# Performance work log

Measured on AMD Instinct MI355X. Metric: run time of the kernel, lower is better.

The kernel has to match this reference:

```python
import jax, jax.numpy as jnp
import numpy as np

TQ, TV, B, D, UNITS = 256, 1024, 4, 128, 128
NEG_INF = -1e9


def setup_inputs() -> dict:
    key = jax.random.key(0)
    k1, k2, k3, k4, k5, k6 = jax.random.split(key, 6)
    query = jax.random.normal(k1, (TQ, B, D), dtype=jnp.float32)
    value = jax.random.normal(k2, (TV, B, D), dtype=jnp.float32)
    mask = jax.random.randint(k3, (TV, B), 0, 2).astype(bool)
    # guarantee at least one valid key position per batch element
    mask = mask.at[0].set(True)
    # Dense kernels (glorot-uniform-like scaled normals are fine for a reference)
    W1 = jax.random.normal(k4, (D, UNITS), dtype=jnp.float32) * (1.0 / np.sqrt(D))
    W2 = jax.random.normal(k5, (D, UNITS), dtype=jnp.float32) * (1.0 / np.sqrt(D))
    # AdditiveAttention use_scale=True -> learnable scale vector of shape (units,)
    scale = jax.random.normal(k6, (UNITS,), dtype=jnp.float32) * (1.0 / np.sqrt(UNITS))
    return {"query": query, "value": value, "mask": mask, "W1": W1, "W2": W2, "scale": scale}


def reference(query, value, mask, W1, W2, scale):
    # time-major -> batch-major
    q = jnp.transpose(query, (1, 0, 2))   # [B, Tq, D]
    v = jnp.transpose(value, (1, 0, 2))   # [B, Tv, D]
    m = jnp.transpose(mask, (1, 0))       # [B, Tv] bool (value mask)

    wq = jnp.einsum('bqd,du->bqu', q, W1)  # [B, Tq, U]
    wk = jnp.einsum('bvd,du->bvu', v, W2)  # [B, Tv, U]

    # additive score: sum_u scale[u] * tanh(wq[b,q,u] + wk[b,v,u]) -> [B, Tq, Tv]
    scores = jnp.einsum('u,bqvu->bqv', scale, jnp.tanh(wq[:, :, None, :] + wk[:, None, :, :]))

    scores = jnp.where(m[:, None, :], scores, NEG_INF)
    attn = jax.nn.softmax(scores, axis=-1)          # [B, Tq, Tv]
    ctx = jnp.einsum('bqv,bvd->bqd', attn, v)       # [B, Tq, D]

    # batch-major -> time-major
    return jnp.transpose(ctx, (1, 0, 2))            # [Tq, B, D]
```

## Files before the change

kernel.cpp:

```cpp
#include <hip/hip_runtime.h>


#define TQ 256
#define TV 1024
#define BB 4
#define DD 128
#define UU 128
#define NEG_INF -1e9f
#define C2LOG2E 2.8853900817779268f

__global__ __launch_bounds__(256) void compact_kernel(
    const int* __restrict__ mask,
    const float* __restrict__ scale,
    int* __restrict__ valid_idx,
    int* __restrict__ nvalid,
    float* __restrict__ Ssum)
{
    const int b = blockIdx.x;
    const int t = threadIdx.x, lane = t & 63, wid = t >> 6;
    __shared__ int wsum[4];
    __shared__ float sred[2];

    int m[4];
#pragma unroll
    for (int k = 0; k < 4; ++k) m[k] = mask[(4 * t + k) * BB + b] ? 1 : 0;
    int cnt = m[0] + m[1] + m[2] + m[3];

    int pre = cnt;
#pragma unroll
    for (int off = 1; off < 64; off <<= 1) {
        int y = __shfl_up(pre, off, 64);
        if (lane >= off) pre += y;
    }
    if (lane == 63) wsum[wid] = pre;

    float sv_ = (t < UU) ? scale[t] : 0.f;
#pragma unroll
    for (int off = 32; off > 0; off >>= 1) sv_ += __shfl_xor(sv_, off, 64);
    if (t == 0)  sred[0] = sv_;
    if (t == 64) sred[1] = sv_;
    __syncthreads();

    int base = 0;
#pragma unroll
    for (int w = 0; w < 4; ++w) if (w < wid) base += wsum[w];
    int total = wsum[0] + wsum[1] + wsum[2] + wsum[3];
    int idx = base + pre - cnt;

#pragma unroll
    for (int k = 0; k < 4; ++k)
        if (m[k]) valid_idx[b * TV + (idx++)] = 4 * t + k;
    for (int i = t; i < TV; i += 256)
        if (i >= total) valid_idx[b * TV + i] = 0;
    if (t == 0) nvalid[b] = total;
    if (b == 0 && t == 0) Ssum[0] = sred[0] + sred[1];
}

__global__ __launch_bounds__(256) void proj_all_kernel(
    const float* __restrict__ query, const float* __restrict__ value,
    const float* __restrict__ W1, const float* __restrict__ W2,
    float* __restrict__ Eq, float* __restrict__ Ek)
{
    __shared__ float Wl[DD * UU];
    __shared__ float xs[8][DD];
    const int t = threadIdx.x;

    const bool isq = blockIdx.x < (TQ * BB / 8);
    const float* X = isq ? query : value;
    const float* W = isq ? W1 : W2;
    float* out     = isq ? Eq : Ek;
    const int T    = isq ? TQ : TV;
    const int R0   = (isq ? blockIdx.x : blockIdx.x - TQ * BB / 8) * 8;

    {
        const float4* Wg = (const float4*)W;
        float4* Wl4 = (float4*)Wl;
#pragma unroll
        for (int k = 0; k < 16; ++k)
            Wl4[k * 256 + t] = Wg[k * 256 + t];
        ((float4*)xs)[t] = ((const float4*)(X + (size_t)R0 * DD))[t];
    }
    __syncthreads();

    const int half = t >> 7;
    const int u = t & 127;
    float a[4] = {0.f, 0.f, 0.f, 0.f};
#pragma unroll 4
    for (int d = 0; d < DD; ++d) {
        float wv = Wl[d * UU + u];
#pragma unroll
        for (int i = 0; i < 4; ++i)
            a[i] += xs[half * 4 + i][d] * wv;
    }
#pragma unroll
    for (int i = 0; i < 4; ++i) {
        int rf = R0 + half * 4 + i;
        int b = rf & (BB - 1), tt = rf >> 2;
        out[((size_t)b * T + tt) * UU + u] =
            __builtin_amdgcn_exp2f(a[i] * C2LOG2E);
    }
}

__global__ __launch_bounds__(256) void scores_kernel(
    const float* __restrict__ Eq,
    const float* __restrict__ Ek,
    const float* __restrict__ scale,
    const float* __restrict__ Ssum,
    const int*   __restrict__ valid_idx,
    const int*   __restrict__ nvalid,
    float* __restrict__ scores)
{
    const int b  = blockIdx.z;
    const int nv = nvalid[b];
    const int v0 = blockIdx.x * 64;
    if (v0 >= nv) return;
    const int q0 = blockIdx.y * 16;
    const int t  = threadIdx.x;

    __shared__ float4 eq_lds[16 * 32];
    __shared__ float4 ek_lds[64 * 32];
    __shared__ int    vidx[64];

    if (t < 64) vidx[t] = valid_idx[b * TV + v0 + t];
    {
        const float4* g = (const float4*)Eq + ((size_t)(b * TQ + q0)) * 32;
        eq_lds[t]       = g[t];
        eq_lds[256 + t] = g[256 + t];
    }
    __syncthreads();
    {
        const float4* g = (const float4*)Ek;
#pragma unroll
        for (int k = 0; k < 8; ++k) {
            int i = k * 256 + t;
            int r = i >> 5, c = i & 31;
            ek_lds[r * 32 + (c ^ (r & 7))] =
                g[((size_t)(b * TV + vidx[r])) * 32 + c];
        }
    }
    __syncthreads();

    const int qp = t >> 5;
    const int vp = t & 31;
    const int sx = vp & 7;
    const float4* Ar0 = eq_lds + (2 * qp) * 32;
    const float4* Ar1 = Ar0 + 32;
    const float4* Kr0 = ek_lds + vp * 32;
    const float4* Kr1 = ek_lds + (vp + 32) * 32;
    const float4* S4  = (const float4*)scale;

    float a00 = 0.f, a01 = 0.f, a10 = 0.f, a11 = 0.f;

#define PAIR(Acomp, Kvec, svc, accA, accB)                           \
    {                                                                \
        float d0 = __builtin_fmaf(A0.Acomp, Kvec.Acomp, 1.f);        \
        float d1 = __builtin_fmaf(A1.Acomp, Kvec.Acomp, 1.f);        \
        float R  = __builtin_amdgcn_rcpf(d0 * d1);                   \
        accA = __builtin_fmaf(svc, R * d1, accA);                    \
        accB = __builtin_fmaf(svc, R * d0, accB);                    \
    }

#pragma unroll 8
    for (int uu = 0; uu < 32; ++uu) {
        float4 A0 = Ar0[uu];
        float4 A1 = Ar1[uu];
        int cs = uu ^ sx;
        float4 K0 = Kr0[cs];
        float4 K1 = Kr1[cs];
        float4 sv = S4[uu];
        PAIR(x, K0, sv.x, a00, a10)
        PAIR(y, K0, sv.y, a00, a10)
        PAIR(z, K0, sv.z, a00, a10)
        PAIR(w, K0, sv.w, a00, a10)
        PAIR(x, K1, sv.x, a01, a11)
        PAIR(y, K1, sv.y, a01, a11)
        PAIR(z, K1, sv.z, a01, a11)
        PAIR(w, K1, sv.w, a01, a11)
    }
#undef PAIR

    const float S = Ssum[0];
    float* row0 = scores + ((size_t)(b * TQ + q0 + 2 * qp)) * TV + v0;
    row0[vp]           = __builtin_fmaf(-2.f, a00, S);
    row0[vp + 32]      = __builtin_fmaf(-2.f, a01, S);
    row0[TV + vp]      = __builtin_fmaf(-2.f, a10, S);
    row0[TV + vp + 32] = __builtin_fmaf(-2.f, a11, S);
}

__global__ __launch_bounds__(512) void softmax_ctx_kernel(
    const float* __restrict__ value,
    const int*   __restrict__ valid_idx,
    const int*   __restrict__ nvalid,
    const float* __restrict__ scores,
    float* __restrict__ out)
{
    const int bi = blockIdx.x;
    const int b  = bi >> 6;
    const int q0 = (bi & 63) * 4;
    const int nv = nvalid[b];
    const int t = threadIdx.x, lane = t & 63;

    __shared__ float p_lds[4][TV];
    __shared__ int   vidx[TV];
    __shared__ float redm[4][2];
    __shared__ float reds[4][2];
    __shared__ float part[3][4][DD];

    if (t < 256) ((int4*)vidx)[t] = ((const int4*)(valid_idx + b * TV))[t];

    const int j = t >> 7;
    const int c = t & 127;
    const int wslot = (t >> 6) & 1;

    const float* srow = scores + ((size_t)(b * TQ + q0 + j)) * TV;
    float4 x0 = ((const float4*)srow)[c];
    float4 x1 = ((const float4*)srow)[c + 128];
    const int e0 = 4 * c, e1 = 512 + 4 * c;
    x0.x = (e0 + 0 < nv) ? x0.x : NEG_INF;
    x0.y = (e0 + 1 < nv) ? x0.y : NEG_INF;
    x0.z = (e0 + 2 < nv) ? x0.z : NEG_INF;
    x0.w = (e0 + 3 < nv) ? x0.w : NEG_INF;
    x1.x = (e1 + 0 < nv) ? x1.x : NEG_INF;
    x1.y = (e1 + 1 < nv) ? x1.y : NEG_INF;
    x1.z = (e1 + 2 < nv) ? x1.z : NEG_INF;
    x1.w = (e1 + 3 < nv) ? x1.w : NEG_INF;

    float mm = fmaxf(fmaxf(fmaxf(x0.x, x0.y), fmaxf(x0.z, x0.w)),
                     fmaxf(fmaxf(x1.x, x1.y), fmaxf(x1.z, x1.w)));
#pragma unroll
    for (int off = 32; off > 0; off >>= 1)
        mm = fmaxf(mm, __shfl_xor(mm, off, 64));
    if (lane == 0) redm[j][wslot] = mm;
    __syncthreads();
    mm = fmaxf(redm[j][0], redm[j][1]);

    float4 p0, p1;
    p0.x = __expf(x0.x - mm); p0.y = __expf(x0.y - mm);
    p0.z = __expf(x0.z - mm); p0.w = __expf(x0.w - mm);
    p1.x = __expf(x1.x - mm); p1.y = __expf(x1.y - mm);
    p1.z = __expf(x1.z - mm); p1.w = __expf(x1.w - mm);
    ((float4*)&p_lds[j][0])[c]       = p0;
    ((float4*)&p_lds[j][0])[c + 128] = p1;

    float ss = ((p0.x + p0.y) + (p0.z + p0.w)) +
               ((p1.x + p1.y) + (p1.z + p1.w));
#pragma unroll
    for (int off = 32; off > 0; off >>= 1)
        ss += __shfl_xor(ss, off, 64);
    if (lane == 0) reds[j][wslot] = ss;
    __syncthreads();

    const int qtr = t >> 7;
    const int d = t & 127;
    float acc[4] = {0.f, 0.f, 0.f, 0.f};
    const float* vbase = value + b * DD + d;
#pragma unroll 8
    for (int i = qtr; i < nv; i += 4) {
        float vv = vbase[(size_t)vidx[i] * BB * DD];
#pragma unroll
        for (int jj = 0; jj < 4; ++jj)
            acc[jj] += p_lds[jj][i] * vv;
    }
    if (qtr) {
#pragma unroll
        for (int jj = 0; jj < 4; ++jj) part[qtr - 1][jj][d] = acc[jj];
    }
    __syncthreads();
    if (qtr == 0) {
#pragma unroll
        for (int jj = 0; jj < 4; ++jj) {
            float tot = acc[jj] + part[0][jj][d] + part[1][jj][d] + part[2][jj][d];
            float invj = 1.f / (reds[jj][0] + reds[jj][1]);
            out[((size_t)(q0 + jj) * BB + b) * DD + d] = tot * invj;
        }
    }
}

extern "C" void kernel_launch(void* const* d_in, const int* in_sizes, int n_in,
                              void* d_out, int out_size, void* d_ws, size_t ws_size,
                              hipStream_t stream) {
    const float* query = (const float*)d_in[0];
    const float* value = (const float*)d_in[1];
    const int*   mask  = (const int*)  d_in[2];
    const float* W1    = (const float*)d_in[3];
    const float* W2    = (const float*)d_in[4];
    const float* scale = (const float*)d_in[5];
    float* out = (float*)d_out;

    float* Eq      = (float*)d_ws;
    float* Ek      = Eq + (size_t)BB * TQ * UU;
    float* scores  = Ek + (size_t)BB * TV * UU;
    int*   vidx    = (int*)(scores + (size_t)BB * TQ * TV);
    int*   nvalid  = vidx + BB * TV;
    float* Ssum    = (float*)(nvalid + BB);

    compact_kernel<<<BB, 256, 0, stream>>>(mask, scale, vidx, nvalid, Ssum);
    proj_all_kernel<<<(TQ * BB + TV * BB) / 8, 256, 0, stream>>>(
        query, value, W1, W2, Eq, Ek);
    scores_kernel<<<dim3(TV / 64, TQ / 16, BB), 256, 0, stream>>>(
        Eq, Ek, scale, Ssum, vidx, nvalid, scores);
    softmax_ctx_kernel<<<BB * TQ / 4, 512, 0, stream>>>(
        value, vidx, nvalid, scores, out);
}
```

Baseline: 48.59 us.

## Merge compaction into projection kernel, share reciprocal across four units, vectorize ctx gather

Folds the mask-compaction kernel into the projection kernel as extra blocks, removing one launch. The scores inner loop now shares one reciprocal across four units instead of two (a product of four denominators). This means fewer rcp instructions, at some risk of overflow or precision loss in that product. The softmax-context loop now reads indices and probabilities as float4 chunks and issues four independent gathers per iteration. Scores also gets a launch-bounds occupancy hint.

```diff
diff --git a/kernel.cpp b/kernel.cpp
--- a/kernel.cpp
+++ b/kernel.cpp
@@ -9,99 +9,105 @@
 #define NEG_INF -1e9f
 #define C2LOG2E 2.8853900817779268f
 
-__global__ __launch_bounds__(256) void compact_kernel(
-    const int* __restrict__ mask,
-    const float* __restrict__ scale,
-    int* __restrict__ valid_idx,
-    int* __restrict__ nvalid,
+union SharedA {
+  struct { float Wl[DD * UU]; float xs[8][DD]; } pj;
+  struct { int wsum[4]; float sred[2]; } cp;
+};
+
+__global__ __launch_bounds__(256) void prep_kernel(
+    const float* __restrict__ query, const float* __restrict__ value,
+    const float* __restrict__ W1, const float* __restrict__ W2,
+    const int* __restrict__ mask, const float* __restrict__ scale,
+    float* __restrict__ Eq, float* __restrict__ Ek,
+    int* __restrict__ valid_idx, int* __restrict__ nvalid,
     float* __restrict__ Ssum)
 {
-    const int b = blockIdx.x;
-    const int t = threadIdx.x, lane = t & 63, wid = t >> 6;
-    __shared__ int wsum[4];
-    __shared__ float sred[2];
-
+  __shared__ SharedA u;
+  const int t = threadIdx.x, lane = t & 63, wid = t >> 6;
+  const int bid = blockIdx.x;
+
+  if (bid < BB) {
+    const int b = bid;
     int m[4];
 #pragma unroll
     for (int k = 0; k < 4; ++k) m[k] = mask[(4 * t + k) * BB + b] ? 1 : 0;
     int cnt = m[0] + m[1] + m[2] + m[3];
-
     int pre = cnt;
 #pragma unroll
     for (int off = 1; off < 64; off <<= 1) {
-        int y = __shfl_up(pre, off, 64);
-        if (lane >= off) pre += y;
-    }
-    if (lane == 63) wsum[wid] = pre;
-
+      int y = __shfl_up(pre, off, 64);
+      if (lane >= off) pre += y;
+    }
+    if (lane == 63) u.cp.wsum[wid] = pre;
     float sv_ = (t < UU) ? scale[t] : 0.f;
 #pragma unroll
     for (int off = 32; off > 0; off >>= 1) sv_ += __shfl_xor(sv_, off, 64);
-    if (t == 0)  sred[0] = sv_;
-    if (t == 64) sred[1] = sv_;
+    if (t == 0)  u.cp.sred[0] = sv_;
+    if (t == 64) u.cp.sred[1] = sv_;
     __syncthreads();
-
     int base = 0;
 #pragma unroll
-    for (int w = 0; w < 4; ++w) if (w < wid) base += wsum[w];
-    int total = wsum[0] + wsum[1] + wsum[2] + wsum[3];
+    for (int w = 0; w < 4; ++w) if (w < wid) base += u.cp.wsum[w];
+    int total = u.cp.wsum[0] + u.cp.wsum[1] + u.cp.wsum[2] + u.cp.wsum[3];
     int idx = base + pre - cnt;
-
 #pragma unroll
     for (int k = 0; k < 4; ++k)
-        if (m[k]) valid_idx[b * TV + (idx++)] = 4 * t + k;
+      if (m[k]) valid_idx[b * TV + (idx++)] = 4 * t + k;
     for (int i = t; i < TV; i += 256)
-        if (i >= total) valid_idx[b * TV + i] = 0;
+      if (i >= total) valid_idx[b * TV + i] = 0;
     if (t == 0) nvalid[b] = total;
-    if (b == 0 && t == 0) Ssum[0] = sred[0] + sred[1];
-}
-
-__global__ __launch_bounds__(256) void proj_all_kernel(
-    const float* __restrict__ query, const float* __restrict__ value,
-    const float* __restrict__ W1, const float* __restrict__ W2,
-    float* __restrict__ Eq, float* __restrict__ Ek)
-{
-    __shared__ float Wl[DD * UU];
-    __shared__ float xs[8][DD];
-    const int t = threadIdx.x;
-
-    const bool isq = blockIdx.x < (TQ * BB / 8);
+    if (b == 0 && t == 0) Ssum[0] = u.cp.sred[0] + u.cp.sred[1];
+  } else {
+    const int blk = bid - BB;
+    const bool isq = blk < (TQ * BB / 8);
     const float* X = isq ? query : value;
     const float* W = isq ? W1 : W2;
-    float* out     = isq ? Eq : Ek;
+    float* E       = isq ? Eq : Ek;
     const int T    = isq ? TQ : TV;
-    const int R0   = (isq ? blockIdx.x : blockIdx.x - TQ * BB / 8) * 8;
-
-    {
-        const float4* Wg = (const float4*)W;
-        float4* Wl4 = (float4*)Wl;
-#pragma unroll
-        for (int k = 0; k < 16; ++k)
-            Wl4[k * 256 + t] = Wg[k * 256 + t];
-        ((float4*)xs)[t] = ((const float4*)(X + (size_t)R0 * DD))[t];
-    }
+    const int R0   = (isq ? blk : blk - TQ * BB / 8) * 8;
+
+    const float4* Wg = (const float4*)W;
+    float4* Wl4 = (float4*)u.pj.Wl;
+#pragma unroll
+    for (int k = 0; k < 16; ++k)
+      Wl4[k * 256 + t] = Wg[k * 256 + t];
+    ((float4*)u.pj.xs)[t] = ((const float4*)(X + (size_t)R0 * DD))[t];
     __syncthreads();
 
     const int half = t >> 7;
-    const int u = t & 127;
+    const int uu_ = t & 127;
     float a[4] = {0.f, 0.f, 0.f, 0.f};
 #pragma unroll 4
     for (int d = 0; d < DD; ++d) {
-        float wv = Wl[d * UU + u];
-#pragma unroll
-        for (int i = 0; i < 4; ++i)
-            a[i] += xs[half * 4 + i][d] * wv;
+      float wv = u.pj.Wl[d * UU + uu_];
+#pragma unroll
+      for (int i = 0; i < 4; ++i)
+        a[i] += u.pj.xs[half * 4 + i][d] * wv;
     }
 #pragma unroll
     for (int i = 0; i < 4; ++i) {
-        int rf = R0 + half * 4 + i;
-        int b = rf & (BB - 1), tt = rf >> 2;
-        out[((size_t)b * T + tt) * UU + u] =
-            __builtin_amdgcn_exp2f(a[i] * C2LOG2E);
-    }
+      int rf = R0 + half * 4 + i;
+      int b2 = rf & (BB - 1), tt = rf >> 2;
+      E[((size_t)b2 * T + tt) * UU + uu_] =
+          __builtin_amdgcn_exp2f(a[i] * C2LOG2E);
+    }
+  }
 }
 
-__global__ __launch_bounds__(256) void scores_kernel(
+#define QUAD(Av, Kv, acc)                                          \
+  { float d0 = __builtin_fmaf(Av.x, Kv.x, 1.f);                    \
+    float d1 = __builtin_fmaf(Av.y, Kv.y, 1.f);                    \
+    float d2 = __builtin_fmaf(Av.z, Kv.z, 1.f);                    \
+    float d3 = __builtin_fmaf(Av.w, Kv.w, 1.f);                    \
+    float m01 = d0 * d1, m23 = d2 * d3;                            \
+    float R = __builtin_amdgcn_rcpf(m01 * m23);                    \
+    float q01 = R * m23, q23 = R * m01;                            \
+    acc = __builtin_fmaf(sv.x, q01 * d1, acc);                     \
+    acc = __builtin_fmaf(sv.y, q01 * d0, acc);                     \
+    acc = __builtin_fmaf(sv.z, q23 * d3, acc);                     \
+    acc = __builtin_fmaf(sv.w, q23 * d2, acc); }
+
+__global__ __launch_bounds__(256, 4) void scores_kernel(
     const float* __restrict__ Eq,
     const float* __restrict__ Ek,
     const float* __restrict__ scale,
@@ -110,81 +116,65 @@
     const int*   __restrict__ nvalid,
     float* __restrict__ scores)
 {
-    const int b  = blockIdx.z;
-    const int nv = nvalid[b];
-    const int v0 = blockIdx.x * 64;
-    if (v0 >= nv) return;
-    const int q0 = blockIdx.y * 16;
-    const int t  = threadIdx.x;
-
-    __shared__ float4 eq_lds[16 * 32];
-    __shared__ float4 ek_lds[64 * 32];
-    __shared__ int    vidx[64];
-
-    if (t < 64) vidx[t] = valid_idx[b * TV + v0 + t];
-    {
-        const float4* g = (const float4*)Eq + ((size_t)(b * TQ + q0)) * 32;
-        eq_lds[t]       = g[t];
-        eq_lds[256 + t] = g[256 + t];
-    }
-    __syncthreads();
-    {
-        const float4* g = (const float4*)Ek;
-#pragma unroll
-        for (int k = 0; k < 8; ++k) {
-            int i = k * 256 + t;
-            int r = i >> 5, c = i & 31;
-            ek_lds[r * 32 + (c ^ (r & 7))] =
-                g[((size_t)(b * TV + vidx[r])) * 32 + c];
-        }
-    }
-    __syncthreads();
-
-    const int qp = t >> 5;
-    const int vp = t & 31;
-    const int sx = vp & 7;
-    const float4* Ar0 = eq_lds + (2 * qp) * 32;
-    const float4* Ar1 = Ar0 + 32;
-    const float4* Kr0 = ek_lds + vp * 32;
-    const float4* Kr1 = ek_lds + (vp + 32) * 32;
-    const float4* S4  = (const float4*)scale;
-
-    float a00 = 0.f, a01 = 0.f, a10 = 0.f, a11 = 0.f;
-
-#define PAIR(Acomp, Kvec, svc, accA, accB)                           \
-    {                                                                \
-        float d0 = __builtin_fmaf(A0.Acomp, Kvec.Acomp, 1.f);        \
-        float d1 = __builtin_fmaf(A1.Acomp, Kvec.Acomp, 1.f);        \
-        float R  = __builtin_amdgcn_rcpf(d0 * d1);                   \
-        accA = __builtin_fmaf(svc, R * d1, accA);                    \
-        accB = __builtin_fmaf(svc, R * d0, accB);                    \
-    }
-
+  const int b  = blockIdx.z;
+  const int nv = nvalid[b];
+  const int v0 = blockIdx.x * 64;
+  if (v0 >= nv) return;
+  const int q0 = blockIdx.y * 16;
+  const int t  = threadIdx.x;
+
+  __shared__ float4 eq_lds[16 * 32];
+  __shared__ float4 ek_lds[64 * 32];
+  __shared__ int    vidx[64];
+
+  if (t < 64) vidx[t] = valid_idx[b * TV + v0 + t];
+  {
+    const float4* gq = (const float4*)Eq + ((size_t)(b * TQ + q0)) * 32;
+    eq_lds[t]       = gq[t];
+    eq_lds[256 + t] = gq[256 + t];
+  }
+  __syncthreads();
+  {
+    const float4* gk = (const float4*)Ek;
+#pragma unroll
+    for (int k = 0; k < 8; ++k) {
+      int i = k * 256 + t;
+      int r = i >> 5, c = i & 31;
+      ek_lds[r * 32 + (c ^ (r & 7))] =
+          gk[((size_t)(b * TV + vidx[r])) * 32 + c];
+    }
+  }
+  __syncthreads();
+
+  const int qp = t >> 5;
+  const int vp = t & 31;
+  const int sx = vp & 7;
+  const float4* Ar0 = eq_lds + (2 * qp) * 32;
+  const float4* Ar1 = Ar0 + 32;
+  const float4* Kr0 = ek_lds + vp * 32;
+  const float4* Kr1 = ek_lds + (vp + 32) * 32;
+  const float4* S4  = (const float4*)scale;
+
+  float a00 = 0.f, a01 = 0.f, a10 = 0.f, a11 = 0.f;
 #pragma unroll 8
-    for (int uu = 0; uu < 32; ++uu) {
-        float4 A0 = Ar0[uu];
-        float4 A1 = Ar1[uu];
-        int cs = uu ^ sx;
-        float4 K0 = Kr0[cs];
-        float4 K1 = Kr1[cs];
-        float4 sv = S4[uu];
-        PAIR(x, K0, sv.x, a00, a10)
-        PAIR(y, K0, sv.y, a00, a10)
-        PAIR(z, K0, sv.z, a00, a10)
-        PAIR(w, K0, sv.w, a00, a10)
-        PAIR(x, K1, sv.x, a01, a11)
-        PAIR(y, K1, sv.y, a01, a11)
-        PAIR(z, K1, sv.z, a01, a11)
-        PAIR(w, K1, sv.w, a01, a11)
-    }
-#undef PAIR
-
-    const float S = Ssum[0];
-    float* row0 = scores + ((size_t)(b * TQ + q0 + 2 * qp)) * TV + v0;
-    row0[vp]           = __builtin_fmaf(-2.f, a00, S);
-    row0[vp + 32]      = __builtin_fmaf(-2.f, a01, S);
-    row0[TV + vp]      = __builtin_fmaf(-2.f, a10, S);
-    row0[TV + vp + 32] = __builtin_fmaf(-2.f, a11, S);
+  for (int uu = 0; uu < 32; ++uu) {
+    float4 A0 = Ar0[uu];
+    float4 A1 = Ar1[uu];
+    int cs = uu ^ sx;
+    float4 K0 = Kr0[cs];
+    float4 K1 = Kr1[cs];
+    float4 sv = S4[uu];
+    QUAD(A0, K0, a00)
+    QUAD(A0, K1, a01)
+    QUAD(A1, K0, a10)
+    QUAD(A1, K1, a11)
+  }
+  const float S = Ssum[0];
+  float* row0 = scores + ((size_t)(b * TQ + q0 + 2 * qp)) * TV + v0;
+  row0[vp]           = __builtin_fmaf(-2.f, a00, S);
+  row0[vp + 32]      = __builtin_fmaf(-2.f, a01, S);
+  row0[TV + vp]      = __builtin_fmaf(-2.f, a10, S);
+  row0[TV + vp + 32] = __builtin_fmaf(-2.f, a11, S);
 }
 
 __global__ __launch_bounds__(512) void softmax_ctx_kernel(
@@ -194,111 +184,126 @@
     const float* __restrict__ scores,
     float* __restrict__ out)
 {
-    const int bi = blockIdx.x;
-    const int b  = bi >> 6;
-    const int q0 = (bi & 63) * 4;
-    const int nv = nvalid[b];
-    const int t = threadIdx.x, lane = t & 63;
-
-    __shared__ float p_lds[4][TV];
-    __shared__ int   vidx[TV];
-    __shared__ float redm[4][2];
-    __shared__ float reds[4][2];
-    __shared__ float part[3][4][DD];
-
-    if (t < 256) ((int4*)vidx)[t] = ((const int4*)(valid_idx + b * TV))[t];
-
-    const int j = t >> 7;
-    const int c = t & 127;
-    const int wslot = (t >> 6) & 1;
-
-    const float* srow = scores + ((size_t)(b * TQ + q0 + j)) * TV;
-    float4 x0 = ((const float4*)srow)[c];
-    float4 x1 = ((const float4*)srow)[c + 128];
-    const int e0 = 4 * c, e1 = 512 + 4 * c;
-    x0.x = (e0 + 0 < nv) ? x0.x : NEG_INF;
-    x0.y = (e0 + 1 < nv) ? x0.y : NEG_INF;
-    x0.z = (e0 + 2 < nv) ? x0.z : NEG_INF;
-    x0.w = (e0 + 3 < nv) ? x0.w : NEG_INF;
-    x1.x = (e1 + 0 < nv) ? x1.x : NEG_INF;
-    x1.y = (e1 + 1 < nv) ? x1.y : NEG_INF;
-    x1.z = (e1 + 2 < nv) ? x1.z : NEG_INF;
-    x1.w = (e1 + 3 < nv) ? x1.w : NEG_INF;
-
-    float mm = fmaxf(fmaxf(fmaxf(x0.x, x0.y), fmaxf(x0.z, x0.w)),
-                     fmaxf(fmaxf(x1.x, x1.y), fmaxf(x1.z, x1.w)));
-#pragma unroll
-    for (int off = 32; off > 0; off >>= 1)
-        mm = fmaxf(mm, __shfl_xor(mm, off, 64));
-    if (lane == 0) redm[j][wslot] = mm;
-    __syncthreads();
-    mm = fmaxf(redm[j][0], redm[j][1]);
-
-    float4 p0, p1;
-    p0.x = __expf(x0.x - mm); p0.y = __expf(x0.y - mm);
-    p0.z = __expf(x0.z - mm); p0.w = __expf(x0.w - mm);
-    p1.x = __expf(x1.x - mm); p1.y = __expf(x1.y - mm);
-    p1.z = __expf(x1.z - mm); p1.w = __expf(x1.w - mm);
-    ((float4*)&p_lds[j][0])[c]       = p0;
-    ((float4*)&p_lds[j][0])[c + 128] = p1;
-
-    float ss = ((p0.x + p0.y) + (p0.z + p0.w)) +
-               ((p1.x + p1.y) + (p1.z + p1.w));
-#pragma unroll
-    for (int off = 32; off > 0; off >>= 1)
-        ss += __shfl_xor(ss, off, 64);
-    if (lane == 0) reds[j][wslot] = ss;
-    __syncthreads();
-
-    const int qtr = t >> 7;
-    const int d = t & 127;
-    float acc[4] = {0.f, 0.f, 0.f, 0.f};
-    const float* vbase = value + b * DD + d;
-#pragma unroll 8
-    for (int i = qtr; i < nv; i += 4) {
-        float vv = vbase[(size_t)vidx[i] * BB * DD];
-#pragma unroll
-        for (int jj = 0; jj < 4; ++jj)
-            acc[jj] += p_lds[jj][i] * vv;
-    }
-    if (qtr) {
-#pragma unroll
-        for (int jj = 0; jj < 4; ++jj) part[qtr - 1][jj][d] = acc[jj];
-    }
-    __syncthreads();
-    if (qtr == 0) {
-#pragma unroll
-        for (int jj = 0; jj < 4; ++jj) {
-            float tot = acc[jj] + part[0][jj][d] + part[1][jj][d] + part[2][jj][d];
-            float invj = 1.f / (reds[jj][0] + reds[jj][1]);
-            out[((size_t)(q0 + jj) * BB + b) * DD + d] = tot * invj;
-        }
-    }
+  const int bi = blockIdx.x;
+  const int b  = bi >> 6;
+  const int q0 = (bi & 63) * 4;
+  const int nv = nvalid[b];
+  const int t = threadIdx.x, lane = t & 63;
+
+  __shared__ float p_lds[4][TV];
+  __shared__ int   vidx[TV];
+  __shared__ float redm[4][2];
+  __shared__ float reds[4][2];
+  __shared__ float part[3][4][DD];
+
+  if (t < 256) ((int4*)vidx)[t] = ((const int4*)(valid_idx + b * TV))[t];
+
+  const int j = t >> 7;
+  const int c = t & 127;
+  const int wslot = (t >> 6) & 1;
+
+  const float* srow = scores + ((size_t)(b * TQ + q0 + j)) * TV;
+  float4 x0 = ((const float4*)srow)[c];
+  float4 x1 = ((const float4*)srow)[c + 128];
+  const int e0 = 4 * c, e1 = 512 + 4 * c;
+  x0.x = (e0 + 0 < nv) ? x0.x : NEG_INF;
+  x0.y = (e0 + 1 < nv) ? x0.y : NEG_INF;
+  x0.z = (e0 + 2 < nv) ? x0.z : NEG_INF;
+  x0.w = (e0 + 3 < nv) ? x0.w : NEG_INF;
+  x1.x = (e1 + 0 < nv) ? x1.x : NEG_INF;
+  x1.y = (e1 + 1 < nv) ? x1.y : NEG_INF;
+  x1.z = (e1 + 2 < nv) ? x1.z : NEG_INF;
+  x1.w = (e1 + 3 < nv) ? x1.w : NEG_INF;
+
+  float mm = fmaxf(fmaxf(fmaxf(x0.x, x0.y), fmaxf(x0.z, x0.w)),
+                   fmaxf(fmaxf(x1.x, x1.y), fmaxf(x1.z, x1.w)));
+#pragma unroll
+  for (int off = 32; off > 0; off >>= 1)
+    mm = fmaxf(mm, __shfl_xor(mm, off, 64));
+  if (lane == 0) redm[j][wslot] = mm;
+  __syncthreads();
+  mm = fmaxf(redm[j][0], redm[j][1]);
+
+  float4 p0, p1;
+  p0.x = __expf(x0.x - mm); p0.y = __expf(x0.y - mm);
+  p0.z = __expf(x0.z - mm); p0.w = __expf(x0.w - mm);
+  p1.x = __expf(x1.x - mm); p1.y = __expf(x1.y - mm);
+  p1.z = __expf(x1.z - mm); p1.w = __expf(x1.w - mm);
+  ((float4*)&p_lds[j][0])[c]       = p0;
+  ((float4*)&p_lds[j][0])[c + 128] = p1;
+
+  float ss = ((p0.x + p0.y) + (p0.z + p0.w)) +
+             ((p1.x + p1.y) + (p1.z + p1.w));
+#pragma unroll
+  for (int off = 32; off > 0; off >>= 1)
+    ss += __shfl_xor(ss, off, 64);
+  if (lane == 0) reds[j][wslot] = ss;
+  __syncthreads();
+
+  const int qtr = t >> 7;
+  const int d = t & 127;
+  const int nChunks = (nv + 3) >> 2;
+  float a0 = 0.f, a1 = 0.f, a2 = 0.f, a3 = 0.f;
+  const float* vbase = value + b * DD + d;
+  for (int ch = qtr; ch < nChunks; ch += 4) {
+    int4 id = ((const int4*)vidx)[ch];
+    float4 q0v = ((const float4*)&p_lds[0][0])[ch];
+    float4 q1v = ((const float4*)&p_lds[1][0])[ch];
+    float4 q2v = ((const float4*)&p_lds[2][0])[ch];
+    float4 q3v = ((const float4*)&p_lds[3][0])[ch];
+    float v0_ = vbase[(size_t)id.x * (BB * DD)];
+    float v1_ = vbase[(size_t)id.y * (BB * DD)];
+    float v2_ = vbase[(size_t)id.z * (BB * DD)];
+    float v3_ = vbase[(size_t)id.w * (BB * DD)];
+    a0 = __builtin_fmaf(q0v.x, v0_, a0); a0 = __builtin_fmaf(q0v.y, v1_, a0);
+    a0 = __builtin_fmaf(q0v.z, v2_, a0); a0 = __builtin_fmaf(q0v.w, v3_, a0);
+    a1 = __builtin_fmaf(q1v.x, v0_, a1); a1 = __builtin_fmaf(q1v.y, v1_, a1);
+    a1 = __builtin_fmaf(q1v.z, v2_, a1); a1 = __builtin_fmaf(q1v.w, v3_, a1);
+    a2 = __builtin_fmaf(q2v.x, v0_, a2); a2 = __builtin_fmaf(q2v.y, v1_, a2);
+    a2 = __builtin_fmaf(q2v.z, v2_, a2); a2 = __builtin_fmaf(q2v.w, v3_, a2);
+    a3 = __builtin_fmaf(q3v.x, v0_, a3); a3 = __builtin_fmaf(q3v.y, v1_, a3);
+    a3 = __builtin_fmaf(q3v.z, v2_, a3); a3 = __builtin_fmaf(q3v.w, v3_, a3);
+  }
+  if (qtr) {
+    part[qtr - 1][0][d] = a0;
+    part[qtr - 1][1][d] = a1;
+    part[qtr - 1][2][d] = a2;
+    part[qtr - 1][3][d] = a3;
+  }
+  __syncthreads();
+  if (qtr == 0) {
+    float tot[4] = {a0, a1, a2, a3};
+#pragma unroll
+    for (int jj = 0; jj < 4; ++jj) {
+      float s = tot[jj] + part[0][jj][d] + part[1][jj][d] + part[2][jj][d];
+      float iv = 1.f / (reds[jj][0] + reds[jj][1]);
+      out[((size_t)(q0 + jj) * BB + b) * DD + d] = s * iv;
+    }
+  }
 }
 
 extern "C" void kernel_launch(void* const* d_in, const int* in_sizes, int n_in,
                               void* d_out, int out_size, void* d_ws, size_t ws_size,
                               hipStream_t stream) {
-    const float* query = (const float*)d_in[0];
-    const float* value = (const float*)d_in[1];
-    const int*   mask  = (const int*)  d_in[2];
-    const float* W1    = (const float*)d_in[3];
-    const float* W2    = (const float*)d_in[4];
-    const float* scale = (const float*)d_in[5];
-    float* out = (float*)d_out;
-
-    float* Eq      = (float*)d_ws;
-    float* Ek      = Eq + (size_t)BB * TQ * UU;
-    float* scores  = Ek + (size_t)BB * TV * UU;
-    int*   vidx    = (int*)(scores + (size_t)BB * TQ * TV);
-    int*   nvalid  = vidx + BB * TV;
-    float* Ssum    = (float*)(nvalid + BB);
-
-    compact_kernel<<<BB, 256, 0, stream>>>(mask, scale, vidx, nvalid, Ssum);
-    proj_all_kernel<<<(TQ * BB + TV * BB) / 8, 256, 0, stream>>>(
-        query, value, W1, W2, Eq, Ek);
-    scores_kernel<<<dim3(TV / 64, TQ / 16, BB), 256, 0, stream>>>(
-        Eq, Ek, scale, Ssum, vidx, nvalid, scores);
-    softmax_ctx_kernel<<<BB * TQ / 4, 512, 0, stream>>>(
-        value, vidx, nvalid, scores, out);
+  const float* query = (const float*)d_in[0];
+  const float* value = (const float*)d_in[1];
+  const int*   mask  = (const int*)  d_in[2];
+  const float* W1    = (const float*)d_in[3];
+  const float* W2    = (const float*)d_in[4];
+  const float* scale = (const float*)d_in[5];
+  float* out = (float*)d_out;
+
+  float* Eq      = (float*)d_ws;
+  float* Ek      = Eq + (size_t)BB * TQ * UU;
+  float* scores  = Ek + (size_t)BB * TV * UU;
+  int*   vidx    = (int*)(scores + (size_t)BB * TQ * TV);
+  int*   nvalid  = vidx + BB * TV;
+  float* Ssum    = (float*)(nvalid + BB);
+
+  prep_kernel<<<BB + (TQ + TV) * BB / 8, 256, 0, stream>>>(
+      query, value, W1, W2, mask, scale, Eq, Ek, vidx, nvalid, Ssum);
+  scores_kernel<<<dim3(TV / 64, TQ / 16, BB), 256, 0, stream>>>(
+      Eq, Ek, scale, Ssum, vidx, nvalid, scores);
+  softmax_ctx_kernel<<<BB * TQ / 4, 512, 0, stream>>>(
+      value, vidx, nvalid, scores, out);
 }
```

After: 45.08 us. 1.08x faster.
